# Performance work log

Measured on AMD Instinct MI355X. Metric: run time of the kernel, lower is better.

The kernel has to match this reference:

```python
import jax, jax.numpy as jnp
import numpy as np

LEVELS = 2
BASE_BLOCK = (16, 16)
MAX_DIST = 8
IMG = (1024, 1024)


def _to_blocks(x, bh, bw):
    # [N,C,H,W] -> [BX,BY,N,C,bh,bw]
    N, C, H, W = x.shape
    BX, BY = H // bh, W // bw
    return x.reshape(N, C, BX, bh, BY, bw).transpose(2, 4, 0, 1, 3, 5)


def _from_blocks(b):
    # [BX,BY,N,C,bh,bw] -> [N,C,H,W]
    BX, BY, N, C, bh, bw = b.shape
    return b.transpose(2, 3, 0, 4, 1, 5).reshape(N, C, BX * bh, BY * bw)


def _level_best(ref_b, tgt_b, centers, d):
    # ref_b/tgt_b: [BX,BY,N,C,bh,bw]; centers: [BX,BY,2] candidate-window centers
    BX, BY = ref_b.shape[:2]
    dr = jnp.arange(-d, d + 1)
    offs = jnp.stack(jnp.meshgrid(dr, dr, indexing='ij'), -1).reshape(-1, 2)  # [K,2] lexicographic (dx,dy)
    hi = jnp.array([BX - 1, BY - 1])

    def step(carry, off):
        cand = centers + off  # [BX,BY,2]
        valid = jnp.all((cand >= 0) & (cand <= hi), axis=-1)
        cc = jnp.clip(cand, 0, hi)
        g = tgt_b[cc[..., 0], cc[..., 1]]  # [BX,BY,N,C,bh,bw]
        cost = jnp.mean(jnp.abs(ref_b - g), axis=(2, 3, 4, 5))  # MAD over N,C,h,w
        return carry, jnp.where(valid, cost, jnp.inf)

    _, costs = jax.lax.scan(step, None, offs)  # [K,BX,BY]
    k = jnp.argmin(costs, axis=0)  # first-min tie-break, deterministic
    return centers + offs[k]  # [BX,BY,2] absolute best target-block indices


def reference(reference_frame, target_frame):
    N, C, H, W = reference_frame.shape
    centers = None
    best = None
    tgt_b = None
    BX = BY = 0
    for level in range(LEVELS):
        s = 2 ** (LEVELS - level - 1)
        bh, bw = BASE_BLOCK[0] * s, BASE_BLOCK[1] * s
        BX, BY = H // bh, W // bw
        d = MAX_DIST // (2 ** level)
        ref_b = _to_blocks(reference_frame, bh, bw)
        tgt_b = _to_blocks(target_frame, bh, bw)
        if level == 0:
            gx, gy = jnp.meshgrid(jnp.arange(BX), jnp.arange(BY), indexing='ij')
            centers = jnp.stack([gx, gy], -1)
        best = _level_best(ref_b, tgt_b, centers, d)
        if level < LEVELS - 1:
            # all 4 children inherit window centered at 2*parent_best
            centers = jnp.repeat(jnp.repeat(2 * best, 2, axis=0), 2, axis=1)
    gx, gy = jnp.meshgrid(jnp.arange(BX), jnp.arange(BY), indexing='ij')
    grid = jnp.stack([gx, gy], -1)
    mv = (best - grid).transpose(2, 0, 1)[None].astype(reference_frame.dtype)
    motion_vectors = jnp.broadcast_to(mv, (N, 2, BX, BY))
    pred_b = tgt_b[best[..., 0], best[..., 1]]  # [BX,BY,N,C,bh,bw]
    predicted_frame = _from_blocks(pred_b)
    return motion_vectors, predicted_frame


def setup_inputs() -> dict:
    key = jax.random.key(0)
    k1, k2 = jax.random.split(key)
    N, C = 4, 3
    H, W = IMG
    reference_frame = jax.random.uniform(k1, (N, C, H, W), dtype=jnp.float32)
    target_frame = jax.random.uniform(k2, (N, C, H, W), dtype=jnp.float32)
    return {"reference_frame": reference_frame, "target_frame": target_frame}
```

## Files before the change

### kernel.cpp

```cpp
#include <hip/hip_runtime.h>

#define IMG_W 1024
#define SLICE 1048576
#define INF_F __builtin_huge_valf()

template <int CTRL>
__device__ __forceinline__ float dpp_add_step(float x) {
    int m = __builtin_amdgcn_update_dpp(0, __builtin_bit_cast(int, x), CTRL, 0xf, 0xf, true);
    return x + __builtin_bit_cast(float, m);
}
__device__ __forceinline__ float wave_sum63(float x) {
    x = dpp_add_step<0x111>(x);
    x = dpp_add_step<0x112>(x);
    x = dpp_add_step<0x114>(x);
    x = dpp_add_step<0x118>(x);
    x = dpp_add_step<0x142>(x);
    x = dpp_add_step<0x143>(x);
    return x;
}

typedef const float __attribute__((address_space(1))) gfloat;
typedef float __attribute__((address_space(3))) sfloat;

__global__ __launch_bounds__(256, 2) void hbma_l0(const float* __restrict__ ref,
                                                  const float* __restrict__ tgt,
                                                  float* __restrict__ cost) {
    const int tx  = blockIdx.x;
    const int byo = blockIdx.y;
    const int dxp = blockIdx.z;
    const int di0 = dxp * 2;
    const int ndi = (di0 + 1 < 17) ? 2 : 1;
    const int t = threadIdx.x, lane = t & 63, w = t >> 6;
    const int by = byo * 4 + w;
    const int prow = lane >> 3, pcol = (lane & 7) << 2;
    const int ty0 = byo * 4 - 8;

    bool rvalid[2]; int bxv[2];
    #pragma unroll
    for (int d = 0; d < 2; ++d) {
        const int bx = tx - (di0 + d - 8);
        bxv[d] = bx;
        rvalid[d] = (d < ndi) && ((unsigned)bx < 32u);
    }
    if (!rvalid[0] && !rvalid[1]) return;

    __shared__ float tile[20 * 1024];

    float acc[2][17];
    #pragma unroll
    for (int d = 0; d < 2; ++d)
        #pragma unroll
        for (int y = 0; y < 17; ++y) acc[d][y] = 0.f;

    const int srr = t >> 3, scc = (t & 7) << 2;

    for (int plane = 0; plane < 12; ++plane) {
        const float* tgt_p = tgt + (size_t)plane * SLICE;
        const float* ref_p = ref + (size_t)plane * SLICE;

        __syncthreads();
        #pragma unroll
        for (int i = 0; i < 20; ++i) {
            const int ty = ty0 + i;
            if ((unsigned)ty < 32u) {
                __builtin_amdgcn_global_load_lds(
                    (gfloat*)(tgt_p + (size_t)(tx * 32 + srr) * IMG_W + ty * 32 + scc),
                    (sfloat*)&tile[(i * 256 + t) * 4], 16, 0, 0);
            }
        }
        __syncthreads();

        float4 rf[2][4];
        #pragma unroll
        for (int d = 0; d < 2; ++d)
            if (rvalid[d]) {
                const float* rb = ref_p + (size_t)(bxv[d] * 32 + prow) * IMG_W + by * 32 + pcol;
                #pragma unroll
                for (int i = 0; i < 4; ++i)
                    rf[d][i] = *(const float4*)(rb + (size_t)i * 8 * IMG_W);
            }

        #pragma unroll
        for (int yi = 0; yi < 17; ++yi) {
            const int ty = by + yi - 8;
            if ((unsigned)ty < 32u) {
                const int tb = (ty - ty0) * 1024 + prow * 32 + pcol;
                float4 tv[4];
                #pragma unroll
                for (int i = 0; i < 4; ++i) tv[i] = *(const float4*)&tile[tb + i * 256];
                #pragma unroll
                for (int d = 0; d < 2; ++d)
                    if (rvalid[d]) {
                        float4 a = {0.f, 0.f, 0.f, 0.f};
                        #pragma unroll
                        for (int i = 0; i < 4; ++i) {
                            a.x += __builtin_fabsf(rf[d][i].x - tv[i].x);
                            a.y += __builtin_fabsf(rf[d][i].y - tv[i].y);
                            a.z += __builtin_fabsf(rf[d][i].z - tv[i].z);
                            a.w += __builtin_fabsf(rf[d][i].w - tv[i].w);
                        }
                        acc[d][yi] += (a.x + a.y) + (a.z + a.w);
                    }
            }
        }
    }

    #pragma unroll
    for (int d = 0; d < 2; ++d)
        if (rvalid[d]) {
            #pragma unroll
            for (int yi = 0; yi < 17; ++yi) {
                const int ty = by + yi - 8;
                if ((unsigned)ty < 32u) {
                    const float s = wave_sum63(acc[d][yi]);
                    if (lane == 63)
                        cost[((size_t)bxv[d] * 32 + by) * 289 + (size_t)(di0 + d) * 17 + yi] = s;
                }
            }
        }
}

__global__ __launch_bounds__(256) void hbma_l1(const float* __restrict__ ref,
                                               const float* __restrict__ tgt,
                                               const float* __restrict__ cost,
                                               float* __restrict__ out) {
    const int pid = blockIdx.y * 32 + blockIdx.x;
    const int pbx = ((pid & 7) << 2) + ((pid >> 3) >> 5);
    const int pby = (pid >> 3) & 31;
    const int t = threadIdx.x;
    const int lane = t & 63, w = t >> 6;

    __shared__ float partials[4][81][4];
    __shared__ int2 sbest[4];
    __shared__ float pm_c[4];
    __shared__ int pm_k[4];

    float bc = INF_F; int bk = 1 << 30;
    {
        const float* crow = cost + ((size_t)pbx * 32 + pby) * 289;
        for (int k = t; k < 289; k += 256) {
            const int dx = k / 17 - 8, dy = k % 17 - 8;
            if ((unsigned)(pbx + dx) < 32u && (unsigned)(pby + dy) < 32u) {
                const float c = crow[k];
                if (c < bc) { bc = c; bk = k; }
            }
        }
        #pragma unroll
        for (int o = 32; o > 0; o >>= 1) {
            const float oc = __shfl_down(bc, o, 64);
            const int   ok = __shfl_down(bk, o, 64);
            if (oc < bc || (oc == bc && ok < bk)) { bc = oc; bk = ok; }
        }
        if (lane == 0) { pm_c[w] = bc; pm_k[w] = bk; }
        __syncthreads();
        bc = pm_c[0]; bk = pm_k[0];
        #pragma unroll
        for (int j = 1; j < 4; ++j) {
            const float oc = pm_c[j]; const int ok = pm_k[j];
            if (oc < bc || (oc == bc && ok < bk)) { bc = oc; bk = ok; }
        }
    }
    const int cx = 2 * (pbx + bk / 17 - 8);
    const int cy = 2 * (pby + bk % 17 - 8);

    int off[3];
    #pragma unroll
    for (int i = 0; i < 3; ++i) {
        const int e4 = t + 256 * i;
        const int nc = e4 >> 6;
        const int ww = e4 & 63;
        off[i] = nc * SLICE + (ww >> 2) * IMG_W + ((ww & 3) << 2);
    }
    int cbase[4];
    float4 rf[4][3];
    #pragma unroll
    for (int c = 0; c < 4; ++c) {
        const int bx = 2 * pbx + (c >> 1), by = 2 * pby + (c & 1);
        cbase[c] = (bx * 16) * IMG_W + by * 16;
        #pragma unroll
        for (int i = 0; i < 3; ++i)
            rf[c][i] = *(const float4*)(ref + cbase[c] + off[i]);
    }

    auto issue = [&](int k, float4 (&tv)[3]) -> bool {
        const int ttx = cx + k / 9 - 4;
        const int tty = cy + k % 9 - 4;
        const bool valid = ((unsigned)ttx < 64u) && ((unsigned)tty < 64u);
        if (valid) {
            const float* tb = tgt + (ttx * 16) * IMG_W + tty * 16;
            #pragma unroll
            for (int i = 0; i < 3; ++i) tv[i] = *(const float4*)(tb + off[i]);
        }
        return valid;
    };
    auto compute = [&](int k, const float4 (&tv)[3], bool valid) {
        if (k >= 81) return;
        if (valid) {
            #pragma unroll
            for (int c = 0; c < 4; ++c) {
                float4 a = {0.f, 0.f, 0.f, 0.f};
                #pragma unroll
                for (int i = 0; i < 3; ++i) {
                    a.x += __builtin_fabsf(rf[c][i].x - tv[i].x);
                    a.y += __builtin_fabsf(rf[c][i].y - tv[i].y);
                    a.z += __builtin_fabsf(rf[c][i].z - tv[i].z);
                    a.w += __builtin_fabsf(rf[c][i].w - tv[i].w);
                }
                const float s = wave_sum63((a.x + a.y) + (a.z + a.w));
                if (lane == 63) partials[c][k][w] = s;
            }
        } else if (lane == 63) {
            #pragma unroll
            for (int c = 0; c < 4; ++c) partials[c][k][w] = INF_F;
        }
    };

    float4 tvA[3], tvB[3];
    bool vA = issue(0, tvA);
    for (int k = 0; k < 81; k += 2) {
        const bool vB = (k + 1 < 81) && issue(k + 1, tvB);
        compute(k, tvA, vA);
        const bool vA2 = (k + 2 < 81) && issue(k + 2, tvA);
        compute(k + 1, tvB, vB);
        vA = vA2;
    }
    __syncthreads();

    {
        const int c = w;
        float cbc = INF_F; int cbk = 1 << 30;
        for (int k = lane; k < 81; k += 64) {
            const float4 p4 = *(const float4*)&partials[c][k][0];
            const float cst = (p4.x + p4.y) + (p4.z + p4.w);
            if (cst < cbc) { cbc = cst; cbk = k; }
        }
        #pragma unroll
        for (int o = 32; o > 0; o >>= 1) {
            const float oc = __shfl_down(cbc, o, 64);
            const int   ok = __shfl_down(cbk, o, 64);
            if (oc < cbc || (oc == cbc && ok < cbk)) { cbc = oc; cbk = ok; }
        }
        if (lane == 0) sbest[c] = make_int2(cx + cbk / 9 - 4, cy + cbk % 9 - 4);
    }
    __syncthreads();

    if (t < 32) {
        const int c = t >> 3, n = (t >> 1) & 3, ch = t & 1;
        const int bx = 2 * pbx + (c >> 1), by = 2 * pby + (c & 1);
        const int2 fb = sbest[c];
        out[((n * 2 + ch) * 64 + bx) * 64 + by] = (ch == 0) ? (float)(fb.x - bx) : (float)(fb.y - by);
    }

    float* pred = out + 32768;
    #pragma unroll
    for (int c = 0; c < 4; ++c) {
        const int2 fb = sbest[c];
        const float* sb = tgt + (fb.x * 16) * IMG_W + fb.y * 16;
        float* db = pred + cbase[c];
        #pragma unroll
        for (int i = 0; i < 3; ++i)
            *(float4*)(db + off[i]) = *(const float4*)(sb + off[i]);
    }
}

extern "C" void kernel_launch(void* const* d_in, const int* in_sizes, int n_in,
                              void* d_out, int out_size, void* d_ws, size_t ws_size,
                              hipStream_t stream) {
    const float* ref = (const float*)d_in[0];
    const float* tgt = (const float*)d_in[1];
    float* out = (float*)d_out;

    float* cost = (float*)d_ws;

    hbma_l0<<<dim3(32, 8, 9), 256, 0, stream>>>(ref, tgt, cost);
    hbma_l1<<<dim3(32, 32), 256, 0, stream>>>(ref, tgt, cost, out);
}
```

Before: 604.7 us.

## Retile level-0 search over 4 dx by half dy range; triple-buffer level-1 loads

The level-0 kernel now gives each block 4 horizontal displacements and half of the vertical displacement range instead of 2 displacements and the full range. Each loaded target tile row is reused across more reference blocks, the LDS tile shrinks from 20 to 12 rows, and the occupancy hint rises to 3 blocks per CU. The level-1 kernel moves from double to triple buffering of candidate target loads so more loads are in flight. In exchange, overlapping vertical rows are loaded twice across the dy halves, reference registers grow, and register pressure may cap occupancy.

Result: slower. 1.004 ms (+65.9%).

```diff
diff --git a/kernel.cpp b/kernel.cpp
--- a/kernel.cpp
+++ b/kernel.cpp
@@ -22,35 +22,41 @@
 typedef const float __attribute__((address_space(1))) gfloat;
 typedef float __attribute__((address_space(3))) sfloat;
 
-__global__ __launch_bounds__(256, 2) void hbma_l0(const float* __restrict__ ref,
+__global__ __launch_bounds__(256, 3) void hbma_l0(const float* __restrict__ ref,
                                                   const float* __restrict__ tgt,
                                                   float* __restrict__ cost) {
     const int tx  = blockIdx.x;
     const int byo = blockIdx.y;
-    const int dxp = blockIdx.z;
-    const int di0 = dxp * 2;
-    const int ndi = (di0 + 1 < 17) ? 2 : 1;
+    const int dxq = blockIdx.z >> 1;
+    const int dyh = blockIdx.z & 1;
+    const int di0 = dxq * 4;
+    const int ndi = (dxq == 4) ? 1 : 4;
     const int t = threadIdx.x, lane = t & 63, w = t >> 6;
-    const int by = byo * 4 + w;
+    const int by0 = byo * 4;
+    const int by  = by0 + w;
     const int prow = lane >> 3, pcol = (lane & 7) << 2;
-    const int ty0 = byo * 4 - 8;
-
-    bool rvalid[2]; int bxv[2];
-    #pragma unroll
-    for (int d = 0; d < 2; ++d) {
+    const int dy0 = dyh ? 0 : -8;
+    const int nyi = dyh ? 9 : 8;
+    const int ty0 = by0 + dy0;
+
+    bool rvalid[4]; int bxv[4];
+    bool any = false;
+    #pragma unroll
+    for (int d = 0; d < 4; ++d) {
         const int bx = tx - (di0 + d - 8);
         bxv[d] = bx;
         rvalid[d] = (d < ndi) && ((unsigned)bx < 32u);
-    }
-    if (!rvalid[0] && !rvalid[1]) return;
-
-    __shared__ float tile[20 * 1024];
-
-    float acc[2][17];
-    #pragma unroll
-    for (int d = 0; d < 2; ++d)
-        #pragma unroll
-        for (int y = 0; y < 17; ++y) acc[d][y] = 0.f;
+        any = any || rvalid[d];
+    }
+    if (!any) return;
+
+    __shared__ float tile[12 * 1024];
+
+    float acc[4][9];
+    #pragma unroll
+    for (int d = 0; d < 4; ++d)
+        #pragma unroll
+        for (int y = 0; y < 9; ++y) acc[d][y] = 0.f;
 
     const int srr = t >> 3, scc = (t & 7) << 2;
 
@@ -60,7 +66,7 @@
 
         __syncthreads();
         #pragma unroll
-        for (int i = 0; i < 20; ++i) {
+        for (int i = 0; i < 12; ++i) {
             const int ty = ty0 + i;
             if ((unsigned)ty < 32u) {
                 __builtin_amdgcn_global_load_lds(
@@ -70,9 +76,9 @@
         }
         __syncthreads();
 
-        float4 rf[2][4];
-        #pragma unroll
-        for (int d = 0; d < 2; ++d)
+        float4 rf[4][4];
+        #pragma unroll
+        for (int d = 0; d < 4; ++d)
             if (rvalid[d]) {
                 const float* rb = ref_p + (size_t)(bxv[d] * 32 + prow) * IMG_W + by * 32 + pcol;
                 #pragma unroll
@@ -81,42 +87,46 @@
             }
 
         #pragma unroll
-        for (int yi = 0; yi < 17; ++yi) {
-            const int ty = by + yi - 8;
-            if ((unsigned)ty < 32u) {
-                const int tb = (ty - ty0) * 1024 + prow * 32 + pcol;
-                float4 tv[4];
-                #pragma unroll
-                for (int i = 0; i < 4; ++i) tv[i] = *(const float4*)&tile[tb + i * 256];
-                #pragma unroll
-                for (int d = 0; d < 2; ++d)
-                    if (rvalid[d]) {
-                        float4 a = {0.f, 0.f, 0.f, 0.f};
-                        #pragma unroll
-                        for (int i = 0; i < 4; ++i) {
-                            a.x += __builtin_fabsf(rf[d][i].x - tv[i].x);
-                            a.y += __builtin_fabsf(rf[d][i].y - tv[i].y);
-                            a.z += __builtin_fabsf(rf[d][i].z - tv[i].z);
-                            a.w += __builtin_fabsf(rf[d][i].w - tv[i].w);
+        for (int yi = 0; yi < 9; ++yi) {
+            if (yi < nyi) {
+                const int ty = by + dy0 + yi;
+                if ((unsigned)ty < 32u) {
+                    const int tb = (w + yi) * 1024 + prow * 32 + pcol;
+                    float4 tv[4];
+                    #pragma unroll
+                    for (int i = 0; i < 4; ++i) tv[i] = *(const float4*)&tile[tb + i * 256];
+                    #pragma unroll
+                    for (int d = 0; d < 4; ++d)
+                        if (rvalid[d]) {
+                            float4 a = {0.f, 0.f, 0.f, 0.f};
+                            #pragma unroll
+                            for (int i = 0; i < 4; ++i) {
+                                a.x += __builtin_fabsf(rf[d][i].x - tv[i].x);
+                                a.y += __builtin_fabsf(rf[d][i].y - tv[i].y);
+                                a.z += __builtin_fabsf(rf[d][i].z - tv[i].z);
+                                a.w += __builtin_fabsf(rf[d][i].w - tv[i].w);
+                            }
+                            acc[d][yi] += (a.x + a.y) + (a.z + a.w);
                         }
-                        acc[d][yi] += (a.x + a.y) + (a.z + a.w);
+                }
+            }
+        }
+    }
+
+    #pragma unroll
+    for (int d = 0; d < 4; ++d)
+        if (rvalid[d]) {
+            #pragma unroll
+            for (int yi = 0; yi < 9; ++yi)
+                if (yi < nyi) {
+                    const int ty = by + dy0 + yi;
+                    if ((unsigned)ty < 32u) {
+                        const float s = wave_sum63(acc[d][yi]);
+                        if (lane == 63)
+                            cost[((size_t)bxv[d] * 32 + by) * 289 +
+                                 (size_t)(di0 + d) * 17 + (dy0 + yi + 8)] = s;
                     }
-            }
-        }
-    }
-
-    #pragma unroll
-    for (int d = 0; d < 2; ++d)
-        if (rvalid[d]) {
-            #pragma unroll
-            for (int yi = 0; yi < 17; ++yi) {
-                const int ty = by + yi - 8;
-                if ((unsigned)ty < 32u) {
-                    const float s = wave_sum63(acc[d][yi]);
-                    if (lane == 63)
-                        cost[((size_t)bxv[d] * 32 + by) * 289 + (size_t)(di0 + d) * 17 + yi] = s;
                 }
-            }
         }
 }
 
@@ -194,7 +204,6 @@
         return valid;
     };
     auto compute = [&](int k, const float4 (&tv)[3], bool valid) {
-        if (k >= 81) return;
         if (valid) {
             #pragma unroll
             for (int c = 0; c < 4; ++c) {
@@ -215,14 +224,16 @@
         }
     };
 
-    float4 tvA[3], tvB[3];
+    float4 tvA[3], tvB[3], tvC[3];
     bool vA = issue(0, tvA);
-    for (int k = 0; k < 81; k += 2) {
-        const bool vB = (k + 1 < 81) && issue(k + 1, tvB);
+    bool vB = issue(1, tvB);
+    for (int k = 0; k < 81; k += 3) {
+        const bool vC = (k + 2 < 81) && issue(k + 2, tvC);
         compute(k, tvA, vA);
-        const bool vA2 = (k + 2 < 81) && issue(k + 2, tvA);
+        vA = (k + 3 < 81) && issue(k + 3, tvA);
         compute(k + 1, tvB, vB);
-        vA = vA2;
+        vB = (k + 4 < 81) && issue(k + 4, tvB);
+        compute(k + 2, tvC, vC);
     }
     __syncthreads();
 
@@ -272,6 +283,6 @@
 
     float* cost = (float*)d_ws;
 
-    hbma_l0<<<dim3(32, 8, 9), 256, 0, stream>>>(ref, tgt, cost);
+    hbma_l0<<<dim3(32, 8, 10), 256, 0, stream>>>(ref, tgt, cost);
     hbma_l1<<<dim3(32, 32), 256, 0, stream>>>(ref, tgt, cost, out);
 }
```
